# Optimization experiments

Hardware: AMD Instinct MI355X
Metric: run time of the kernel (lower is better)

Reference implementation:

```python
import jax, jax.numpy as jnp
import numpy as np

N = 65536      # flattened tokens
K = 8192       # codebook_size
D = 64         # codebook_dim
DECAY = 0.9
EPS = 1e-05


def setup_inputs() -> dict:
    key = jax.random.key(0)
    k1, k2, k3, k4 = jax.random.split(key, 4)
    z = jax.random.normal(k1, (N, D), dtype=jnp.float32)
    # codebook initialized uniform(-1, 1) in the torch module
    weight = jax.random.uniform(k2, (K, D), dtype=jnp.float32, minval=-1.0, maxval=1.0)
    # EMA state: positive cluster sizes, embed_avg near the codebook
    cluster_size = jax.random.uniform(k3, (K,), dtype=jnp.float32)
    embed_avg = weight + 0.01 * jax.random.normal(k4, (K, D), dtype=jnp.float32)
    return {"z": z, "weight": weight, "cluster_size": cluster_size, "embed_avg": embed_avg}


def reference(z, weight, cluster_size, embed_avg):
    # VectorQuantizer.ema_update: distances -> argmin -> gather -> EMA stats -> weight refresh
    zd = jax.lax.stop_gradient(z)  # torch uses z.detach() for distance/quant_error
    # distance[n,k] = ||z_n||^2 + ||c_k||^2 - 2 z_n . c_k   (addmm pattern)
    dist = (zd * zd).sum(1, keepdims=True) + (weight * weight).sum(1) - 2.0 * (zd @ weight.T)  # [N, K]
    token = jnp.argmin(dist, axis=1)                      # [N]
    embed = weight[token]                                  # gather [N, D]
    quant_error = jnp.mean(((embed - zd) ** 2).sum(1))

    # onehot_probs.sum(0) == per-code counts; onehot.T @ z == segment sum of z
    counts = jax.ops.segment_sum(jnp.ones((zd.shape[0],), zd.dtype), token, num_segments=K)  # [K]
    embed_sum = jax.ops.segment_sum(z, token, num_segments=K)                                # [K, D]

    new_cluster_size = cluster_size * DECAY + (1.0 - DECAY) * counts
    new_embed_avg = embed_avg * DECAY + (1.0 - DECAY) * embed_sum

    # ema_weight_update with num_tokens = codebook_size
    n = new_cluster_size.sum()
    smoothed = (new_cluster_size + EPS) / (n + K * EPS) * n
    new_weight = new_embed_avg / smoothed[:, None]

    return quant_error, new_weight, new_cluster_size, new_embed_avg
```

## Files before the change

kernel.cpp:

```cpp
#include <hip/hip_runtime.h>
#include <type_traits>

#define N_TOK 65536
#define K_CODE 8192
#define D_DIM 64

constexpr float DECAY = 0.9f;
constexpr float OMD = 0.1f;
constexpr float EPS = 1e-5f;

constexpr int OUT_QE = 0;
constexpr int OUT_W  = 1;
constexpr int OUT_CS = 1 + K_CODE * D_DIM;
constexpr int OUT_EA = OUT_CS + K_CODE;

constexpr int WS_QE     = 0;
constexpr int WS_NSUM   = 1;
constexpr int WS_COUNTS = 16;
constexpr int WS_EMBSUM = WS_COUNTS + K_CODE;
constexpr int WS_CNORM  = WS_EMBSUM + K_CODE * D_DIM;
constexpr int WS_WHI    = WS_CNORM + K_CODE;
constexpr int WS_WLO    = WS_WHI + K_CODE * D_DIM / 2;
constexpr int WS_ZERO   = WS_CNORM;

typedef __attribute__((ext_vector_type(16))) float floatx16;
typedef __attribute__((ext_vector_type(8)))  short short8;
typedef __attribute__((ext_vector_type(8)))  __bf16 bf16x8;

template <typename T, typename = void> struct mfma_takes : std::false_type {};
template <typename T>
struct mfma_takes<T, std::void_t<decltype(__builtin_amdgcn_mfma_f32_32x32x16_bf16(
    std::declval<T>(), std::declval<T>(), std::declval<floatx16>(), 0, 0, 0))>>
    : std::true_type {};

__device__ __forceinline__ floatx16 MFMA(short8 a, short8 b, floatx16 c) {
  if constexpr (mfma_takes<bf16x8>::value) {
    return __builtin_amdgcn_mfma_f32_32x32x16_bf16(
        __builtin_bit_cast(bf16x8, a), __builtin_bit_cast(bf16x8, b), c, 0, 0, 0);
  } else {
    return __builtin_amdgcn_mfma_f32_32x32x16_bf16(a, b, c, 0, 0, 0);
  }
}

__device__ __forceinline__ unsigned short bf16rne(float x) {
  unsigned int u = __float_as_uint(x);
  return (unsigned short)((u + 0x7FFFu + ((u >> 16) & 1u)) >> 16);
}

__global__ void vq_prep(const float* __restrict__ w, float* __restrict__ ws) {
  const int tid = threadIdx.x;
  const int lane = tid & 63;
  const int k = blockIdx.x * 4 + (tid >> 6);
  const float v = w[(size_t)k * D_DIM + lane];
  const unsigned short h = bf16rne(v);
  const float hf = __uint_as_float((unsigned int)h << 16);
  const unsigned short l = bf16rne(v - hf);
  unsigned short* whi = (unsigned short*)(ws + WS_WHI);
  unsigned short* wlo = (unsigned short*)(ws + WS_WLO);
  whi[(size_t)k * D_DIM + lane] = h;
  wlo[(size_t)k * D_DIM + lane] = l;
  float s = v * v;
#pragma unroll
  for (int m = 32; m >= 1; m >>= 1) s += __shfl_xor(s, m);
  if (lane == 0) ws[WS_CNORM + k] = s;
}

__global__ __launch_bounds__(256, 2) void vq_argmin(
    const float* __restrict__ z, float* __restrict__ ws)
{
  __shared__ __align__(16) unsigned short Wlds[2][2][32 * 72];
  __shared__ float mind_s[128];
  __shared__ int   tok_s[128];

  const int tid  = threadIdx.x;
  const int w    = tid >> 6;
  const int lane = tid & 63;
  const int m    = lane & 31;
  const int h    = lane >> 5;
  const int tb   = blockIdx.x * 128;

  const unsigned short* whi = (const unsigned short*)(ws + WS_WHI);
  const unsigned short* wlo = (const unsigned short*)(ws + WS_WLO);
  const float* cnorm = ws + WS_CNORM;

  short8 ah[4], al[4];
  float znorm = 0.f;
  {
    const float* zrow = z + (size_t)(tb + w * 32 + m) * D_DIM + 8 * h;
#pragma unroll
    for (int s = 0; s < 4; ++s) {
      const float4 v0 = *(const float4*)(zrow + 16 * s);
      const float4 v1 = *(const float4*)(zrow + 16 * s + 4);
      const float vals[8] = {v0.x, v0.y, v0.z, v0.w, v1.x, v1.y, v1.z, v1.w};
#pragma unroll
      for (int j = 0; j < 8; ++j) {
        const float x = vals[j];
        const unsigned short hb = bf16rne(x);
        const float hf = __uint_as_float((unsigned int)hb << 16);
        const unsigned short lb = bf16rne(x - hf);
        ah[s][j] = (short)hb;
        al[s][j] = (short)lb;
        znorm += x * x;
      }
    }
    znorm += __shfl_xor(znorm, 32);
  }

  const int sr = m;
  const int sg = 2 * w + h;
  uint4 sthi, stlo;
  auto stage_load = [&](int c) {
    const size_t off = ((size_t)(c * 32 + sr)) * D_DIM + sg * 8;
    sthi = *(const uint4*)(whi + off);
    stlo = *(const uint4*)(wlo + off);
  };
  auto stage_write = [&](int c) {
    const int b = c & 1;
    *(uint4*)&Wlds[b][0][sr * 72 + sg * 8] = sthi;
    *(uint4*)&Wlds[b][1][sr * 72 + sg * 8] = stlo;
  };

  float minv[16];
  int   mini[16];
#pragma unroll
  for (int r = 0; r < 16; ++r) { minv[r] = 3.4e38f; mini[r] = 0; }

  const floatx16 kZero = {};

  stage_load(0);
  stage_write(0);
  __syncthreads();

  for (int c = 0; c < K_CODE / 32; ++c) {
    const int b = c & 1;
    const float cn = cnorm[c * 32 + m];
    if (c + 1 < K_CODE / 32) stage_load(c + 1);

    short8 bh[4], bl[4];
#pragma unroll
    for (int s = 0; s < 4; ++s) {
      bh[s] = *(const short8*)&Wlds[b][0][m * 72 + (2 * s + h) * 8];
      bl[s] = *(const short8*)&Wlds[b][1][m * 72 + (2 * s + h) * 8];
    }

    floatx16 a0, a1;
    a0 = MFMA(ah[0], bh[0], kZero);
    a1 = MFMA(al[0], bh[0], kZero);
    a0 = MFMA(ah[1], bh[1], a0);
    a1 = MFMA(al[1], bh[1], a1);
    a0 = MFMA(ah[2], bh[2], a0);
    a1 = MFMA(al[2], bh[2], a1);
    a0 = MFMA(ah[3], bh[3], a0);
    a1 = MFMA(al[3], bh[3], a1);
    a0 = MFMA(ah[0], bl[0], a0);
    a1 = MFMA(ah[2], bl[2], a1);
    a0 = MFMA(ah[1], bl[1], a0);
    a1 = MFMA(ah[3], bl[3], a1);

    const int idxc = c * 32 + m;
#pragma unroll
    for (int r = 0; r < 16; ++r) {
      const float d = __builtin_fmaf(-2.f, a0[r] + a1[r], cn);
      if (d < minv[r]) { minv[r] = d; mini[r] = idxc; }
    }

    if (c + 1 < K_CODE / 32) stage_write(c + 1);
    __syncthreads();
  }

#pragma unroll
  for (int r = 0; r < 16; ++r) {
#pragma unroll
    for (int mm = 1; mm < 32; mm <<= 1) {
      const float ov = __shfl_xor(minv[r], mm);
      const int   oi = __shfl_xor(mini[r], mm);
      if (ov < minv[r] || (ov == minv[r] && oi < mini[r])) { minv[r] = ov; mini[r] = oi; }
    }
  }
#pragma unroll
  for (int r = 0; r < 16; ++r) {
    const int mr = (r & 3) + 8 * (r >> 2) + 4 * h;
    if (m == mr) {
      tok_s[w * 32 + mr]  = mini[r];
      mind_s[w * 32 + mr] = minv[r] + znorm;
    }
  }
  __syncthreads();

  float* counts = ws + WS_COUNTS;
  float* embsum = ws + WS_EMBSUM;

  if (tid < 128) {
    float qe = mind_s[tid];
#pragma unroll
    for (int mm = 32; mm >= 1; mm >>= 1) qe += __shfl_xor(qe, mm);
    if ((tid & 63) == 0) atomicAdd(ws + WS_QE, qe);
    atomicAdd(&counts[tok_s[tid]], 1.0f);
  }

#pragma unroll 4
  for (int t = 0; t < 32; ++t) {
    const int row = w * 32 + t;
    const int tk = tok_s[row];
    const float zv = z[(size_t)(tb + row) * D_DIM + lane];
    atomicAdd(&embsum[(size_t)tk * D_DIM + lane], zv);
  }
}

__global__ void vq_finalize_cs(const float* __restrict__ cluster_size,
                               float* __restrict__ ws, float* __restrict__ out)
{
  const int k = blockIdx.x * 256 + threadIdx.x;
  const float ncs = cluster_size[k] * DECAY + OMD * ws[WS_COUNTS + k];
  out[OUT_CS + k] = ncs;
  float s = ncs;
#pragma unroll
  for (int m = 32; m >= 1; m >>= 1) s += __shfl_xor(s, m);
  __shared__ float part[4];
  if ((threadIdx.x & 63) == 0) part[threadIdx.x >> 6] = s;
  __syncthreads();
  if (threadIdx.x == 0) {
    atomicAdd(ws + WS_NSUM, part[0] + part[1] + part[2] + part[3]);
    if (blockIdx.x == 0) out[OUT_QE] = ws[WS_QE] * (1.0f / N_TOK);
  }
}

__global__ void vq_finalize_w(const float* __restrict__ embed_avg,
                              const float* __restrict__ ws, float* __restrict__ out)
{
  const int idx = blockIdx.x * 256 + threadIdx.x;
  const int k = idx >> 6;
  const float nea = embed_avg[idx] * DECAY + OMD * ws[WS_EMBSUM + idx];
  out[OUT_EA + idx] = nea;
  const float n = ws[WS_NSUM];
  const float ncs = out[OUT_CS + k];
  const float sm = (ncs + EPS) / (n + K_CODE * EPS) * n;
  out[OUT_W + idx] = nea / sm;
}

extern "C" void kernel_launch(void* const* d_in, const int* in_sizes, int n_in,
                              void* d_out, int out_size, void* d_ws, size_t ws_size,
                              hipStream_t stream) {
  const float* z  = (const float*)d_in[0];
  const float* w  = (const float*)d_in[1];
  const float* cs = (const float*)d_in[2];
  const float* ea = (const float*)d_in[3];
  float* out = (float*)d_out;
  float* ws  = (float*)d_ws;

  hipMemsetAsync(d_ws, 0, (size_t)WS_ZERO * sizeof(float), stream);

  vq_prep<<<K_CODE / 4, 256, 0, stream>>>(w, ws);
  vq_argmin<<<N_TOK / 128, 256, 0, stream>>>(z, ws);
  vq_finalize_cs<<<K_CODE / 256, 256, 0, stream>>>(cs, ws, out);
  vq_finalize_w<<<K_CODE * D_DIM / 256, 256, 0, stream>>>(ea, ws, out);
}
```

Before: 310.8 us.

## Fold codebook norm into MFMA and stage 128-code swizzled tiles per block

Result: slower. 365.1 us (+17.5%).

```diff
diff --git a/kernel.cpp b/kernel.cpp
--- a/kernel.cpp
+++ b/kernel.cpp
@@ -18,10 +18,10 @@
 constexpr int WS_NSUM   = 1;
 constexpr int WS_COUNTS = 16;
 constexpr int WS_EMBSUM = WS_COUNTS + K_CODE;
-constexpr int WS_CNORM  = WS_EMBSUM + K_CODE * D_DIM;
-constexpr int WS_WHI    = WS_CNORM + K_CODE;
+constexpr int WS_WHI    = WS_EMBSUM + K_CODE * D_DIM;
 constexpr int WS_WLO    = WS_WHI + K_CODE * D_DIM / 2;
-constexpr int WS_ZERO   = WS_CNORM;
+constexpr int WS_CNP    = WS_WLO + K_CODE * D_DIM / 2;
+constexpr int WS_ZERO   = WS_WHI;
 
 typedef __attribute__((ext_vector_type(16))) float floatx16;
 typedef __attribute__((ext_vector_type(8)))  short short8;
@@ -62,109 +62,134 @@
   float s = v * v;
 #pragma unroll
   for (int m = 32; m >= 1; m >>= 1) s += __shfl_xor(s, m);
-  if (lane == 0) ws[WS_CNORM + k] = s;
-}
-
-__global__ __launch_bounds__(256, 2) void vq_argmin(
+  if (lane == 0) {
+    const float cn2 = 0.5f * s;
+    const unsigned short ch = bf16rne(cn2);
+    const float chf = __uint_as_float((unsigned int)ch << 16);
+    const unsigned short cl = bf16rne(cn2 - chf);
+    ((unsigned int*)(ws + WS_CNP))[k] = (unsigned int)ch | ((unsigned int)cl << 16);
+  }
+}
+
+__global__ __launch_bounds__(512, 2) void vq_argmin(
     const float* __restrict__ z, float* __restrict__ ws)
 {
-  __shared__ __align__(16) unsigned short Wlds[2][2][32 * 72];
-  __shared__ float mind_s[128];
-  __shared__ int   tok_s[128];
+  __shared__ __align__(16) unsigned short Wbuf[2][2][128 * 64];
 
   const int tid  = threadIdx.x;
   const int w    = tid >> 6;
   const int lane = tid & 63;
   const int m    = lane & 31;
   const int h    = lane >> 5;
-  const int tb   = blockIdx.x * 128;
+  const int tb   = blockIdx.x * 256;
 
   const unsigned short* whi = (const unsigned short*)(ws + WS_WHI);
   const unsigned short* wlo = (const unsigned short*)(ws + WS_WLO);
-  const float* cnorm = ws + WS_CNORM;
+  const unsigned int*   cnp = (const unsigned int*)(ws + WS_CNP);
 
   short8 ah[4], al[4];
   float znorm = 0.f;
   {
     const float* zrow = z + (size_t)(tb + w * 32 + m) * D_DIM + 8 * h;
 #pragma unroll
-    for (int s = 0; s < 4; ++s) {
-      const float4 v0 = *(const float4*)(zrow + 16 * s);
-      const float4 v1 = *(const float4*)(zrow + 16 * s + 4);
+    for (int s4 = 0; s4 < 4; ++s4) {
+      const float4 v0 = *(const float4*)(zrow + 16 * s4);
+      const float4 v1 = *(const float4*)(zrow + 16 * s4 + 4);
       const float vals[8] = {v0.x, v0.y, v0.z, v0.w, v1.x, v1.y, v1.z, v1.w};
 #pragma unroll
       for (int j = 0; j < 8; ++j) {
         const float x = vals[j];
-        const unsigned short hb = bf16rne(x);
+        znorm += x * x;
+        const float y = -x;
+        const unsigned short hb = bf16rne(y);
         const float hf = __uint_as_float((unsigned int)hb << 16);
-        const unsigned short lb = bf16rne(x - hf);
-        ah[s][j] = (short)hb;
-        al[s][j] = (short)lb;
-        znorm += x * x;
+        const unsigned short lb = bf16rne(y - hf);
+        ah[s4][j] = (short)hb;
+        al[s4][j] = (short)lb;
       }
     }
     znorm += __shfl_xor(znorm, 32);
   }
 
-  const int sr = m;
-  const int sg = 2 * w + h;
-  uint4 sthi, stlo;
-  auto stage_load = [&](int c) {
-    const size_t off = ((size_t)(c * 32 + sr)) * D_DIM + sg * 8;
-    sthi = *(const uint4*)(whi + off);
-    stlo = *(const uint4*)(wlo + off);
-  };
-  auto stage_write = [&](int c) {
-    const int b = c & 1;
-    *(uint4*)&Wlds[b][0][sr * 72 + sg * 8] = sthi;
-    *(uint4*)&Wlds[b][1][sr * 72 + sg * 8] = stlo;
-  };
+  short8 acn;
+  {
+    uint4 ab = {0u, 0u, 0u, 0u};
+    ab.x = (h == 0) ? 0x3F803F80u : 0u;
+    acn = __builtin_bit_cast(short8, ab);
+  }
+  const floatx16 kZero = {};
 
   float minv[16];
   int   mini[16];
 #pragma unroll
   for (int r = 0; r < 16; ++r) { minv[r] = 3.4e38f; mini[r] = 0; }
 
-  const floatx16 kZero = {};
-
-  stage_load(0);
-  stage_write(0);
+  uint4 sl[4];
+  auto stageLoad = [&](int s) {
+    const unsigned short* bh8 = whi + (size_t)s * (128 * 64);
+    const unsigned short* bl8 = wlo + (size_t)s * (128 * 64);
+#pragma unroll
+    for (int i = 0; i < 2; ++i) {
+      sl[i]     = *(const uint4*)(bh8 + (size_t)(i * 512 + tid) * 8);
+      sl[2 + i] = *(const uint4*)(bl8 + (size_t)(i * 512 + tid) * 8);
+    }
+  };
+  auto stageWrite = [&](int cb) {
+#pragma unroll
+    for (int i = 0; i < 2; ++i) {
+      const int idx = i * 512 + tid;
+      const int r = idx >> 3, g = idx & 7;
+      const int off = r * 64 + ((g ^ (r & 7)) * 8);
+      *(uint4*)&Wbuf[cb][0][off] = sl[i];
+      *(uint4*)&Wbuf[cb][1][off] = sl[2 + i];
+    }
+  };
+
+  stageLoad(0);
+  stageWrite(0);
   __syncthreads();
 
-  for (int c = 0; c < K_CODE / 32; ++c) {
-    const int b = c & 1;
-    const float cn = cnorm[c * 32 + m];
-    if (c + 1 < K_CODE / 32) stage_load(c + 1);
-
-    short8 bh[4], bl[4];
-#pragma unroll
-    for (int s = 0; s < 4; ++s) {
-      bh[s] = *(const short8*)&Wlds[b][0][m * 72 + (2 * s + h) * 8];
-      bl[s] = *(const short8*)&Wlds[b][1][m * 72 + (2 * s + h) * 8];
-    }
-
-    floatx16 a0, a1;
-    a0 = MFMA(ah[0], bh[0], kZero);
-    a1 = MFMA(al[0], bh[0], kZero);
-    a0 = MFMA(ah[1], bh[1], a0);
-    a1 = MFMA(al[1], bh[1], a1);
-    a0 = MFMA(ah[2], bh[2], a0);
-    a1 = MFMA(al[2], bh[2], a1);
-    a0 = MFMA(ah[3], bh[3], a0);
-    a1 = MFMA(al[3], bh[3], a1);
-    a0 = MFMA(ah[0], bl[0], a0);
-    a1 = MFMA(ah[2], bl[2], a1);
-    a0 = MFMA(ah[1], bl[1], a0);
-    a1 = MFMA(ah[3], bl[3], a1);
-
-    const int idxc = c * 32 + m;
-#pragma unroll
-    for (int r = 0; r < 16; ++r) {
-      const float d = __builtin_fmaf(-2.f, a0[r] + a1[r], cn);
-      if (d < minv[r]) { minv[r] = d; mini[r] = idxc; }
-    }
-
-    if (c + 1 < K_CODE / 32) stage_write(c + 1);
+  for (int s = 0; s < 64; ++s) {
+    const int cb = s & 1;
+    if (s + 1 < 64) stageLoad(s + 1);
+
+    const unsigned short* bhb = &Wbuf[cb][0][0];
+    const unsigned short* blb = &Wbuf[cb][1][0];
+
+#pragma unroll 2
+    for (int kc = 0; kc < 4; ++kc) {
+      const int rowoff = (kc * 32 + m) * 64;
+      short8 bh[4], bl[4];
+#pragma unroll
+      for (int s4 = 0; s4 < 4; ++s4) {
+        const int off = rowoff + (((2 * s4 + h) ^ (m & 7)) * 8);
+        bh[s4] = *(const short8*)(bhb + off);
+        bl[s4] = *(const short8*)(blb + off);
+      }
+      const int code = s * 128 + kc * 32 + m;
+      short8 bcn;
+      {
+        uint4 bb = {0u, 0u, 0u, 0u};
+        bb.x = (h == 0) ? cnp[code] : 0u;
+        bcn = __builtin_bit_cast(short8, bb);
+      }
+      floatx16 acc = MFMA(acn, bcn, kZero);
+#pragma unroll
+      for (int s4 = 0; s4 < 4; ++s4) {
+        acc = MFMA(ah[s4], bh[s4], acc);
+        acc = MFMA(al[s4], bh[s4], acc);
+        acc = MFMA(ah[s4], bl[s4], acc);
+      }
+#pragma unroll
+      for (int r = 0; r < 16; ++r) {
+        const float d = acc[r];
+        const bool lt = d < minv[r];
+        minv[r] = lt ? d : minv[r];
+        mini[r] = lt ? code : mini[r];
+      }
+    }
+
+    if (s + 1 < 64) stageWrite(cb ^ 1);
     __syncthreads();
   }
 
@@ -177,12 +202,16 @@
       if (ov < minv[r] || (ov == minv[r] && oi < mini[r])) { minv[r] = ov; mini[r] = oi; }
     }
   }
+
+  float* mind_s = (float*)&Wbuf[0][0][0];
+  int*   tok_s  = (int*)&Wbuf[0][0][0] + 256;
+
 #pragma unroll
   for (int r = 0; r < 16; ++r) {
     const int mr = (r & 3) + 8 * (r >> 2) + 4 * h;
     if (m == mr) {
       tok_s[w * 32 + mr]  = mini[r];
-      mind_s[w * 32 + mr] = minv[r] + znorm;
+      mind_s[w * 32 + mr] = 2.0f * minv[r] + znorm;
     }
   }
   __syncthreads();
@@ -190,7 +219,7 @@
   float* counts = ws + WS_COUNTS;
   float* embsum = ws + WS_EMBSUM;
 
-  if (tid < 128) {
+  if (tid < 256) {
     float qe = mind_s[tid];
 #pragma unroll
     for (int mm = 32; mm >= 1; mm >>= 1) qe += __shfl_xor(qe, mm);
@@ -248,10 +277,10 @@
   float* out = (float*)d_out;
   float* ws  = (float*)d_ws;
 
-  hipMemsetAsync(d_ws, 0, (size_t)WS_ZERO * sizeof(float), stream);
+  (void)hipMemsetAsync(d_ws, 0, (size_t)WS_ZERO * sizeof(float), stream);
 
   vq_prep<<<K_CODE / 4, 256, 0, stream>>>(w, ws);
-  vq_argmin<<<N_TOK / 128, 256, 0, stream>>>(z, ws);
+  vq_argmin<<<N_TOK / 256, 512, 0, stream>>>(z, ws);
   vq_finalize_cs<<<K_CODE / 256, 256, 0, stream>>>(cs, ws, out);
   vq_finalize_w<<<K_CODE * D_DIM / 256, 256, 0, stream>>>(ea, ws, out);
 }
```

## Split codebook across wave pairs with 64-token blocks and single accumulator chain

Applied to the files above, without the earlier changes.

Result: slower. 457.0 us (+47.0%).

```diff
diff --git a/kernel.cpp b/kernel.cpp
--- a/kernel.cpp
+++ b/kernel.cpp
@@ -65,106 +65,110 @@
   if (lane == 0) ws[WS_CNORM + k] = s;
 }
 
-__global__ __launch_bounds__(256, 2) void vq_argmin(
+__global__ __launch_bounds__(256, 4) void vq_argmin(
     const float* __restrict__ z, float* __restrict__ ws)
 {
-  __shared__ __align__(16) unsigned short Wlds[2][2][32 * 72];
-  __shared__ float mind_s[128];
-  __shared__ int   tok_s[128];
+  __shared__ __align__(16) unsigned short Wbuf[2][2][2][32 * 72];
+  __shared__ float mind_s[2][64];
+  __shared__ int   tok_s[2][64];
 
   const int tid  = threadIdx.x;
   const int w    = tid >> 6;
   const int lane = tid & 63;
   const int m    = lane & 31;
   const int h    = lane >> 5;
-  const int tb   = blockIdx.x * 128;
+  const int tg   = w & 1;
+  const int hw   = w >> 1;
+  const int tb   = blockIdx.x * 64;
 
   const unsigned short* whi = (const unsigned short*)(ws + WS_WHI);
   const unsigned short* wlo = (const unsigned short*)(ws + WS_WLO);
-  const float* cnorm = ws + WS_CNORM;
+  const float* cnorm_g = ws + WS_CNORM;
 
   short8 ah[4], al[4];
   float znorm = 0.f;
   {
-    const float* zrow = z + (size_t)(tb + w * 32 + m) * D_DIM + 8 * h;
-#pragma unroll
-    for (int s = 0; s < 4; ++s) {
-      const float4 v0 = *(const float4*)(zrow + 16 * s);
-      const float4 v1 = *(const float4*)(zrow + 16 * s + 4);
+    const float* zrow = z + (size_t)(tb + tg * 32 + m) * D_DIM + 8 * h;
+#pragma unroll
+    for (int s4 = 0; s4 < 4; ++s4) {
+      const float4 v0 = *(const float4*)(zrow + 16 * s4);
+      const float4 v1 = *(const float4*)(zrow + 16 * s4 + 4);
       const float vals[8] = {v0.x, v0.y, v0.z, v0.w, v1.x, v1.y, v1.z, v1.w};
 #pragma unroll
       for (int j = 0; j < 8; ++j) {
         const float x = vals[j];
+        znorm += x * x;
         const unsigned short hb = bf16rne(x);
         const float hf = __uint_as_float((unsigned int)hb << 16);
         const unsigned short lb = bf16rne(x - hf);
-        ah[s][j] = (short)hb;
-        al[s][j] = (short)lb;
-        znorm += x * x;
+        ah[s4][j] = (short)hb;
+        al[s4][j] = (short)lb;
       }
     }
     znorm += __shfl_xor(znorm, 32);
   }
-
-  const int sr = m;
-  const int sg = 2 * w + h;
-  uint4 sthi, stlo;
-  auto stage_load = [&](int c) {
-    const size_t off = ((size_t)(c * 32 + sr)) * D_DIM + sg * 8;
-    sthi = *(const uint4*)(whi + off);
-    stlo = *(const uint4*)(wlo + off);
-  };
-  auto stage_write = [&](int c) {
-    const int b = c & 1;
-    *(uint4*)&Wlds[b][0][sr * 72 + sg * 8] = sthi;
-    *(uint4*)&Wlds[b][1][sr * 72 + sg * 8] = stlo;
-  };
 
   float minv[16];
   int   mini[16];
 #pragma unroll
   for (int r = 0; r < 16; ++r) { minv[r] = 3.4e38f; mini[r] = 0; }
 
+  const int srow = tid >> 3;
+  const int scol = tid & 7;
+  uint4 sl[4];
+  auto stageLoad = [&](int s) {
+    const size_t off0 = ((size_t)(s * 32 + srow)) * D_DIM + scol * 8;
+    const size_t off1 = ((size_t)(4096 + s * 32 + srow)) * D_DIM + scol * 8;
+    sl[0] = *(const uint4*)(whi + off0);
+    sl[1] = *(const uint4*)(wlo + off0);
+    sl[2] = *(const uint4*)(whi + off1);
+    sl[3] = *(const uint4*)(wlo + off1);
+  };
+  auto stageWrite = [&](int b) {
+    const int loff = srow * 72 + scol * 8;
+    *(uint4*)&Wbuf[0][b][0][loff] = sl[0];
+    *(uint4*)&Wbuf[0][b][1][loff] = sl[1];
+    *(uint4*)&Wbuf[1][b][0][loff] = sl[2];
+    *(uint4*)&Wbuf[1][b][1][loff] = sl[3];
+  };
+
+  stageLoad(0);
+  stageWrite(0);
+  __syncthreads();
+
   const floatx16 kZero = {};
 
-  stage_load(0);
-  stage_write(0);
-  __syncthreads();
-
-  for (int c = 0; c < K_CODE / 32; ++c) {
-    const int b = c & 1;
-    const float cn = cnorm[c * 32 + m];
-    if (c + 1 < K_CODE / 32) stage_load(c + 1);
+  for (int s = 0; s < 128; ++s) {
+    const int b = s & 1;
+    const float cn = cnorm_g[hw * 4096 + s * 32 + m];
+    if (s + 1 < 128) stageLoad(s + 1);
 
     short8 bh[4], bl[4];
 #pragma unroll
-    for (int s = 0; s < 4; ++s) {
-      bh[s] = *(const short8*)&Wlds[b][0][m * 72 + (2 * s + h) * 8];
-      bl[s] = *(const short8*)&Wlds[b][1][m * 72 + (2 * s + h) * 8];
-    }
-
-    floatx16 a0, a1;
-    a0 = MFMA(ah[0], bh[0], kZero);
-    a1 = MFMA(al[0], bh[0], kZero);
-    a0 = MFMA(ah[1], bh[1], a0);
-    a1 = MFMA(al[1], bh[1], a1);
-    a0 = MFMA(ah[2], bh[2], a0);
-    a1 = MFMA(al[2], bh[2], a1);
-    a0 = MFMA(ah[3], bh[3], a0);
-    a1 = MFMA(al[3], bh[3], a1);
-    a0 = MFMA(ah[0], bl[0], a0);
-    a1 = MFMA(ah[2], bl[2], a1);
-    a0 = MFMA(ah[1], bl[1], a0);
-    a1 = MFMA(ah[3], bl[3], a1);
-
-    const int idxc = c * 32 + m;
+    for (int s4 = 0; s4 < 4; ++s4) {
+      const int off = m * 72 + (2 * s4 + h) * 8;
+      bh[s4] = *(const short8*)&Wbuf[hw][b][0][off];
+      bl[s4] = *(const short8*)&Wbuf[hw][b][1][off];
+    }
+
+    floatx16 acc = kZero;
+#pragma unroll
+    for (int s4 = 0; s4 < 4; ++s4) acc = MFMA(ah[s4], bh[s4], acc);
+#pragma unroll
+    for (int s4 = 0; s4 < 4; ++s4) acc = MFMA(al[s4], bh[s4], acc);
+#pragma unroll
+    for (int s4 = 0; s4 < 4; ++s4) acc = MFMA(ah[s4], bl[s4], acc);
+
+    const int code = hw * 4096 + s * 32 + m;
 #pragma unroll
     for (int r = 0; r < 16; ++r) {
-      const float d = __builtin_fmaf(-2.f, a0[r] + a1[r], cn);
-      if (d < minv[r]) { minv[r] = d; mini[r] = idxc; }
-    }
-
-    if (c + 1 < K_CODE / 32) stage_write(c + 1);
+      const float d = __builtin_fmaf(-2.f, acc[r], cn);
+      const bool lt = d < minv[r];
+      minv[r] = lt ? d : minv[r];
+      mini[r] = lt ? code : mini[r];
+    }
+
+    if (s + 1 < 128) stageWrite(b ^ 1);
     __syncthreads();
   }
 
@@ -177,12 +181,13 @@
       if (ov < minv[r] || (ov == minv[r] && oi < mini[r])) { minv[r] = ov; mini[r] = oi; }
     }
   }
+
 #pragma unroll
   for (int r = 0; r < 16; ++r) {
     const int mr = (r & 3) + 8 * (r >> 2) + 4 * h;
     if (m == mr) {
-      tok_s[w * 32 + mr]  = mini[r];
-      mind_s[w * 32 + mr] = minv[r] + znorm;
+      tok_s[hw][tg * 32 + mr]  = mini[r];
+      mind_s[hw][tg * 32 + mr] = minv[r] + znorm;
     }
   }
   __syncthreads();
@@ -190,18 +195,25 @@
   float* counts = ws + WS_COUNTS;
   float* embsum = ws + WS_EMBSUM;
 
-  if (tid < 128) {
-    float qe = mind_s[tid];
+  if (tid < 64) {
+    const float d0 = mind_s[0][tid], d1 = mind_s[1][tid];
+    const int   i0 = tok_s[0][tid],  i1 = tok_s[1][tid];
+    const bool t1 = d1 < d0;
+    const float dm = t1 ? d1 : d0;
+    const int   im = t1 ? i1 : i0;
+    tok_s[0][tid] = im;
+    float qe = dm;
 #pragma unroll
     for (int mm = 32; mm >= 1; mm >>= 1) qe += __shfl_xor(qe, mm);
-    if ((tid & 63) == 0) atomicAdd(ws + WS_QE, qe);
-    atomicAdd(&counts[tok_s[tid]], 1.0f);
-  }
+    if (tid == 0) atomicAdd(ws + WS_QE, qe);
+    atomicAdd(&counts[im], 1.0f);
+  }
+  __syncthreads();
 
 #pragma unroll 4
-  for (int t = 0; t < 32; ++t) {
-    const int row = w * 32 + t;
-    const int tk = tok_s[row];
+  for (int t = 0; t < 16; ++t) {
+    const int row = w * 16 + t;
+    const int tk = tok_s[0][row];
     const float zv = z[(size_t)(tb + row) * D_DIM + lane];
     atomicAdd(&embsum[(size_t)tk * D_DIM + lane], zv);
   }
@@ -248,10 +260,10 @@
   float* out = (float*)d_out;
   float* ws  = (float*)d_ws;
 
-  hipMemsetAsync(d_ws, 0, (size_t)WS_ZERO * sizeof(float), stream);
+  (void)hipMemsetAsync(d_ws, 0, (size_t)WS_ZERO * sizeof(float), stream);
 
   vq_prep<<<K_CODE / 4, 256, 0, stream>>>(w, ws);
-  vq_argmin<<<N_TOK / 128, 256, 0, stream>>>(z, ws);
+  vq_argmin<<<N_TOK / 64, 256, 0, stream>>>(z, ws);
   vq_finalize_cs<<<K_CODE / 256, 256, 0, stream>>>(cs, ws, out);
   vq_finalize_w<<<K_CODE * D_DIM / 256, 256, 0, stream>>>(ea, ws, out);
 }
```
